# Kernel tuning notes

Hardware: AMD Instinct MI355X
Metric: run time of the kernel (lower is better)

## Reference

```python
import jax, jax.numpy as jnp
import numpy as np

DIM = 1024; NH = 16; HD = DIM // NH          # head_dim = 64
E = 8; K = 2; TEMP = 1.0; HID = 1024         # routed experts / top-k / moe_inter_dim
SHID = HID * 1                               # shared expert hidden (n_shared_experts=1)
EPS = 1e-6


def _rms(x, w):
    return x * jax.lax.rsqrt(jnp.mean(x * x, axis=-1, keepdims=True) + EPS) * w


def setup_inputs() -> dict:
    key = jax.random.key(0)
    ks = jax.random.split(key, 16)
    B, S = 2, 2048
    x = jax.random.normal(ks[0], (B, S, DIM), jnp.float32)
    # RoPE table: (S, HD//2, 2) with [..., 0]=cos, [..., 1]=sin  (theta=10000)
    inv = 1.0 / (10000.0 ** (jnp.arange(0, HD, 2, dtype=jnp.float32) / HD))
    ang = jnp.arange(S, dtype=jnp.float32)[:, None] * inv[None, :]
    freqs = jnp.stack([jnp.cos(ang), jnp.sin(ang)], axis=-1)
    sc = 0.02
    W = lambda k, shape: jax.random.normal(k, shape, jnp.float32) * sc
    return dict(
        x=x, freqs=freqs,
        att_norm_w=jnp.ones((DIM,), jnp.float32),
        wq=W(ks[1], (DIM, DIM)), wk=W(ks[2], (DIM, DIM)),
        wv=W(ks[3], (DIM, DIM)), wo=W(ks[4], (DIM, DIM)),
        ffn_norm_w=jnp.ones((DIM,), jnp.float32),
        gate_w=W(ks[5], (E, DIM)),
        ew1=W(ks[6], (E, DIM, HID)), ew2=W(ks[7], (E, HID, DIM)), ew3=W(ks[8], (E, DIM, HID)),
        sw1=W(ks[9], (DIM, SHID)), sw2=W(ks[10], (SHID, DIM)), sw3=W(ks[11], (DIM, SHID)),
    )


def reference(x, freqs, att_norm_w, wq, wk, wv, wo, ffn_norm_w, gate_w,
              ew1, ew2, ew3, sw1, sw2, sw3):
    B, S, _ = x.shape
    # --- attention sub-block ---
    xn = _rms(x, att_norm_w)
    q = (xn @ wq).reshape(B, S, NH, HD)
    k = (xn @ wk).reshape(B, S, NH, HD)
    v = (xn @ wv).reshape(B, S, NH, HD)
    cos = freqs[:S, :, 0][None, :, None, :]  # (1,S,1,HD//2)
    sin = freqs[:S, :, 1][None, :, None, :]
    def rope(t):  # complex multiply on interleaved (real, imag) pairs
        t = t.reshape(B, S, NH, HD // 2, 2)
        r = t[..., 0] * cos - t[..., 1] * sin
        i = t[..., 0] * sin + t[..., 1] * cos
        return jnp.stack([r, i], axis=-1).reshape(B, S, NH, HD)
    q = rope(q); k = rope(k)
    q = q.transpose(0, 2, 1, 3); k = k.transpose(0, 2, 1, 3); v = v.transpose(0, 2, 1, 3)
    scores = jnp.einsum('bhqd,bhkd->bhqk', q, k) / np.sqrt(HD).astype(np.float32)
    probs = jax.nn.softmax(scores.astype(jnp.float32), axis=-1).astype(q.dtype)
    att = jnp.einsum('bhqk,bhkd->bhqd', probs, v).transpose(0, 2, 1, 3).reshape(B, S, DIM)
    h = x + att @ wo
    # --- MoE sub-block ---
    hn = _rms(h, ffn_norm_w).reshape(-1, DIM)  # (N, DIM), N = B*S
    N = hn.shape[0]
    gate_scores = (hn @ gate_w.T) / TEMP
    gate_probs = jax.nn.softmax(gate_scores, axis=-1)
    topk_vals, topk_idx = jax.lax.top_k(gate_probs, K)
    # expert_mask[n, e] = routing weight (0 if not in top-k)
    expert_mask = jnp.zeros((N, E), hn.dtype).at[jnp.arange(N)[:, None], topk_idx].set(topk_vals)
    # dense grouped-GEMM form of the per-expert gather/compute/scatter loop;
    # tokens not routed to expert e get weight 0 => identical math
    h1 = jnp.einsum('nd,edh->enh', hn, ew1)
    h3 = jnp.einsum('nd,edh->enh', hn, ew3)
    eo = jnp.einsum('enh,ehd->end', jax.nn.silu(h1) * h3, ew2)
    y = jnp.einsum('end,ne->nd', eo, expert_mask)
    shared = (jax.nn.silu(hn @ sw1) * (hn @ sw3)) @ sw2
    return h + (y + shared).reshape(B, S, DIM)
```

## Files before the change

kernel.cpp:

```cpp
#include <hip/hip_runtime.h>

#define DIMD 1024
#define NHEAD 16
#define HDIM 64
#define SEQ 2048
#define NBATCH 2
#define NTOK 4096
#define NEXP 8
#define HIDD 1024
#define NSLOT 8192
#define MAXTILES 72
#define FA_BQ 128
#define FA_BK 128

typedef unsigned short ushort_t;
typedef __bf16 bf16x8 __attribute__((ext_vector_type(8)));
typedef float f32x4 __attribute__((ext_vector_type(4)));
typedef unsigned short ushort8v __attribute__((ext_vector_type(8)));
typedef unsigned short ushort4v __attribute__((ext_vector_type(4)));

#define GLL16(gp, lp) __builtin_amdgcn_global_load_lds( \
    (const __attribute__((address_space(1))) unsigned int*)(gp), \
    (__attribute__((address_space(3))) unsigned int*)(lp), 16, 0, 0)

__device__ inline float bf2f(ushort_t b) {
    union { unsigned int u; float f; } v; v.u = ((unsigned int)b) << 16; return v.f;
}
__device__ inline ushort_t f2bf(float f) {
    union { float f; unsigned int u; } v; v.f = f;
    unsigned int u = v.u;
    return (ushort_t)((u + 0x7FFFu + ((u >> 16) & 1u)) >> 16);
}
__device__ inline ushort_t cvt_bf16(float f) { return f2bf(f); }
__device__ inline ushort_t cvt_bf16(ushort_t u) { return u; }

template <typename Tin>
__global__ __launch_bounds__(256) void transpose_bf16(
    const Tin* __restrict__ in, ushort_t* __restrict__ out,
    int R, int C, int ld_in, int ld_out, int nb1,
    long si1, long si2, long so1, long so2)
{
    __shared__ ushort_t tile[32][33];
    int z = blockIdx.z, z1 = z % nb1, z2 = z / nb1;
    in  += (size_t)z1 * si1 + (size_t)z2 * si2;
    out += (size_t)z1 * so1 + (size_t)z2 * so2;
    int c0 = blockIdx.x * 32, r0 = blockIdx.y * 32;
    int tx = threadIdx.x & 31, ty = threadIdx.x >> 5;
#pragma unroll
    for (int i = 0; i < 4; i++) {
        int r = r0 + ty + i * 8, c = c0 + tx;
        ushort_t v = 0;
        if (r < R && c < C) v = cvt_bf16(in[(size_t)r * ld_in + c]);
        tile[ty + i * 8][tx] = v;
    }
    __syncthreads();
#pragma unroll
    for (int i = 0; i < 4; i++) {
        int cc = c0 + ty + i * 8, rr = r0 + tx;
        if (cc < C && rr < R) out[(size_t)cc * ld_out + rr] = tile[tx][ty + i * 8];
    }
}

__global__ __launch_bounds__(256) void rmsnorm_kernel(
    const float* __restrict__ x, const float* __restrict__ w, ushort_t* __restrict__ out)
{
    size_t row = blockIdx.x;
    const float* xr = x + row * DIMD;
    int t = threadIdx.x;
    float4 xv = ((const float4*)xr)[t];
    float ss = xv.x * xv.x + xv.y * xv.y + xv.z * xv.z + xv.w * xv.w;
    for (int o = 32; o; o >>= 1) ss += __shfl_xor(ss, o, 64);
    __shared__ float red[4];
    if ((t & 63) == 0) red[t >> 6] = ss;
    __syncthreads();
    ss = red[0] + red[1] + red[2] + red[3];
    float rs = 1.0f / sqrtf(ss / (float)DIMD + 1e-6f);
    float4 wv = ((const float4*)w)[t];
    ushort4v o;
    o[0] = f2bf(xv.x * rs * wv.x); o[1] = f2bf(xv.y * rs * wv.y);
    o[2] = f2bf(xv.z * rs * wv.z); o[3] = f2bf(xv.w * rs * wv.w);
    *(ushort4v*)(out + row * DIMD + t * 4) = o;
}

template <bool OUT_BF16, bool RESID>
__global__ __launch_bounds__(256, 2) void gemm_bt(
    const ushort_t* __restrict__ A, const ushort_t* __restrict__ B,
    void* __restrict__ Cv, const float* __restrict__ Rres,
    int M, int N, int K, int lda, int ldb, int ldc,
    int nb1, long sA1, long sA2, long sB1, long sB2, long sC1, long sC2,
    float alpha)
{
    __shared__ ushort_t lsA[128][32];
    __shared__ ushort_t lsB[128][32];
    int z = blockIdx.z, z1 = z % nb1, z2 = z / nb1;
    A += (size_t)z1 * sA1 + (size_t)z2 * sA2;
    B += (size_t)z1 * sB1 + (size_t)z2 * sB2;
    size_t coff = (size_t)z1 * sC1 + (size_t)z2 * sC2;
    int tn0 = blockIdx.x * 128, tm0 = blockIdx.y * 128;
    int t = threadIdx.x;
    int wave = t >> 6, lane = t & 63;
    int wm = (wave >> 1) * 64, wn = (wave & 1) * 64;
    int lrow = lane & 15, quad = lane >> 4;
    char* lsAb = (char*)&lsA[0][0];
    char* lsBb = (char*)&lsB[0][0];
    f32x4 acc[4][4] = {};

    for (int kt = 0; kt < K; kt += 32) {
        __syncthreads();
#pragma unroll
        for (int cc = 0; cc < 2; cc++) {
            int c = t + cc * 256;
            int r = c >> 2, kc = (c & 3) * 8;
            int ar = tm0 + r; ar = (ar < M) ? ar : (M - 1);
            GLL16(A + (size_t)ar * lda + kt + kc, lsAb + (size_t)c * 16);
            int br = tn0 + r; br = (br < N) ? br : (N - 1);
            GLL16(B + (size_t)br * ldb + kt + kc, lsBb + (size_t)c * 16);
        }
        __syncthreads();
        bf16x8 afr[4], bfr[4];
#pragma unroll
        for (int i = 0; i < 4; i++) {
            afr[i] = *(const bf16x8*)(&lsA[wm + i * 16 + lrow][quad * 8]);
            bfr[i] = *(const bf16x8*)(&lsB[wn + i * 16 + lrow][quad * 8]);
        }
#pragma unroll
        for (int mi = 0; mi < 4; mi++)
#pragma unroll
            for (int ni = 0; ni < 4; ni++)
                acc[mi][ni] = __builtin_amdgcn_mfma_f32_16x16x32_bf16(
                    afr[mi], bfr[ni], acc[mi][ni], 0, 0, 0);
    }
#pragma unroll
    for (int mi = 0; mi < 4; mi++)
#pragma unroll
        for (int ni = 0; ni < 4; ni++) {
            int col = tn0 + wn + ni * 16 + lrow;
            if (col >= N) continue;
            int row0 = tm0 + wm + mi * 16 + quad * 4;
#pragma unroll
            for (int r = 0; r < 4; r++) {
                int row = row0 + r;
                if (row >= M) continue;
                size_t idx = coff + (size_t)row * ldc + col;
                float v = acc[mi][ni][r] * alpha;
                if (RESID) v += Rres[idx];
                if (OUT_BF16) ((ushort_t*)Cv)[idx] = f2bf(v);
                else          ((float*)Cv)[idx] = v;
            }
        }
}

__global__ __launch_bounds__(256, 2) void gemm_grouped(
    const ushort_t* __restrict__ A, const ushort_t* __restrict__ Bt,
    ushort_t* __restrict__ C, const int* __restrict__ perm,
    const int* __restrict__ tile_e, const int* __restrict__ tile_r0,
    const int* __restrict__ tile_r1, const int* __restrict__ ntiles, long sBe)
{
    int tt = blockIdx.x;
    if (tt >= *ntiles) return;
    int e = tile_e[tt], r0 = tile_r0[tt], r1 = tile_r1[tt];
    const ushort_t* B = Bt + (size_t)e * sBe;
    int tn0 = blockIdx.y * 128;
    __shared__ ushort_t lsA[128][32];
    __shared__ ushort_t lsB[128][32];
    int t = threadIdx.x;
    int wave = t >> 6, lane = t & 63;
    int wm = (wave >> 1) * 64, wn = (wave & 1) * 64;
    int lrow = lane & 15, quad = lane >> 4;
    char* lsAb = (char*)&lsA[0][0];
    char* lsBb = (char*)&lsB[0][0];
    f32x4 acc[4][4] = {};

    for (int kt = 0; kt < DIMD; kt += 32) {
        __syncthreads();
#pragma unroll
        for (int cc = 0; cc < 2; cc++) {
            int c = t + cc * 256;
            int r = c >> 2, kc = (c & 3) * 8;
            int sl = r0 + r; if (sl >= r1) sl = r1 - 1;
            int ar = perm ? perm[sl] : sl;
            GLL16(A + (size_t)ar * DIMD + kt + kc, lsAb + (size_t)c * 16);
            int br = tn0 + r;
            GLL16(B + (size_t)br * DIMD + kt + kc, lsBb + (size_t)c * 16);
        }
        __syncthreads();
        bf16x8 afr[4], bfr[4];
#pragma unroll
        for (int i = 0; i < 4; i++) {
            afr[i] = *(const bf16x8*)(&lsA[wm + i * 16 + lrow][quad * 8]);
            bfr[i] = *(const bf16x8*)(&lsB[wn + i * 16 + lrow][quad * 8]);
        }
#pragma unroll
        for (int mi = 0; mi < 4; mi++)
#pragma unroll
            for (int ni = 0; ni < 4; ni++)
                acc[mi][ni] = __builtin_amdgcn_mfma_f32_16x16x32_bf16(
                    afr[mi], bfr[ni], acc[mi][ni], 0, 0, 0);
    }
#pragma unroll
    for (int mi = 0; mi < 4; mi++)
#pragma unroll
        for (int ni = 0; ni < 4; ni++) {
            int col = tn0 + wn + ni * 16 + lrow;
            int l0 = wm + mi * 16 + quad * 4;
#pragma unroll
            for (int r = 0; r < 4; r++) {
                int slot = r0 + l0 + r;
                if (slot >= r1) continue;
                C[(size_t)slot * DIMD + col] = f2bf(acc[mi][ni][r]);
            }
        }
}

__global__ __launch_bounds__(256, 2) void moe_mlp1(
    const ushort_t* __restrict__ A, const ushort_t* __restrict__ B1t, const ushort_t* __restrict__ B3t,
    ushort_t* __restrict__ C, const int* __restrict__ perm,
    const int* __restrict__ tile_e, const int* __restrict__ tile_r0,
    const int* __restrict__ tile_r1, const int* __restrict__ ntiles, long sBe)
{
    int tt = blockIdx.x;
    if (tt >= *ntiles) return;
    int e = tile_e[tt], r0 = tile_r0[tt], r1 = tile_r1[tt];
    const ushort_t* B1 = B1t + (size_t)e * sBe;
    const ushort_t* B3 = B3t + (size_t)e * sBe;
    int tn0 = blockIdx.y * 128;
    __shared__ ushort_t lsA[128][32];
    __shared__ ushort_t lsB1[128][32];
    __shared__ ushort_t lsB3[128][32];
    int t = threadIdx.x;
    int wave = t >> 6, lane = t & 63;
    int wm = (wave >> 1) * 64, wn = (wave & 1) * 64;
    int lrow = lane & 15, quad = lane >> 4;
    char* lsAb  = (char*)&lsA[0][0];
    char* lsB1b = (char*)&lsB1[0][0];
    char* lsB3b = (char*)&lsB3[0][0];
    f32x4 acc1[4][4] = {};
    f32x4 acc3[4][4] = {};

    for (int kt = 0; kt < DIMD; kt += 32) {
        __syncthreads();
#pragma unroll
        for (int cc = 0; cc < 2; cc++) {
            int c = t + cc * 256;
            int r = c >> 2, kc = (c & 3) * 8;
            int sl = r0 + r; if (sl >= r1) sl = r1 - 1;
            int ar = perm ? perm[sl] : sl;
            GLL16(A + (size_t)ar * DIMD + kt + kc, lsAb + (size_t)c * 16);
            int br = tn0 + r;
            GLL16(B1 + (size_t)br * DIMD + kt + kc, lsB1b + (size_t)c * 16);
            GLL16(B3 + (size_t)br * DIMD + kt + kc, lsB3b + (size_t)c * 16);
        }
        __syncthreads();
        bf16x8 afr[4], b1fr[4], b3fr[4];
#pragma unroll
        for (int i = 0; i < 4; i++) {
            afr[i]  = *(const bf16x8*)(&lsA[wm + i * 16 + lrow][quad * 8]);
            b1fr[i] = *(const bf16x8*)(&lsB1[wn + i * 16 + lrow][quad * 8]);
            b3fr[i] = *(const bf16x8*)(&lsB3[wn + i * 16 + lrow][quad * 8]);
        }
#pragma unroll
        for (int mi = 0; mi < 4; mi++)
#pragma unroll
            for (int ni = 0; ni < 4; ni++) {
                acc1[mi][ni] = __builtin_amdgcn_mfma_f32_16x16x32_bf16(
                    afr[mi], b1fr[ni], acc1[mi][ni], 0, 0, 0);
                acc3[mi][ni] = __builtin_amdgcn_mfma_f32_16x16x32_bf16(
                    afr[mi], b3fr[ni], acc3[mi][ni], 0, 0, 0);
            }
    }
#pragma unroll
    for (int mi = 0; mi < 4; mi++)
#pragma unroll
        for (int ni = 0; ni < 4; ni++) {
            int col = tn0 + wn + ni * 16 + lrow;
            int l0 = wm + mi * 16 + quad * 4;
#pragma unroll
            for (int r = 0; r < 4; r++) {
                int slot = r0 + l0 + r;
                if (slot >= r1) continue;
                float h1 = acc1[mi][ni][r], h3 = acc3[mi][ni][r];
                float s = h1 / (1.f + __expf(-h1));
                C[(size_t)slot * DIMD + col] = f2bf(s * h3);
            }
        }
}

__global__ __launch_bounds__(256) void rope_kernel(
    const ushort_t* __restrict__ qkv, const float* __restrict__ freqs,
    ushort_t* __restrict__ qout, ushort_t* __restrict__ kout)
{
    int s = blockIdx.x, b = blockIdx.y, t = threadIdx.x;
#pragma unroll
    for (int pp = 0; pp < 2; pp++) {
        int p = t + pp * 256;
        int hh = p >> 5, i = p & 31;
        float cs = freqs[(s * 32 + i) * 2 + 0];
        float sn = freqs[(s * 32 + i) * 2 + 1];
        size_t row = (size_t)(b * SEQ + s) * 3072;
        size_t qi = row + hh * HDIM + 2 * i;
        size_t ki = row + 1024 + hh * HDIM + 2 * i;
        size_t out_idx = ((size_t)((b * NHEAD + hh) * SEQ + s)) * HDIM + 2 * i;
        float t0 = bf2f(qkv[qi]), t1 = bf2f(qkv[qi + 1]);
        qout[out_idx]     = f2bf(t0 * cs - t1 * sn);
        qout[out_idx + 1] = f2bf(t0 * sn + t1 * cs);
        t0 = bf2f(qkv[ki]); t1 = bf2f(qkv[ki + 1]);
        kout[out_idx]     = f2bf(t0 * cs - t1 * sn);
        kout[out_idx + 1] = f2bf(t0 * sn + t1 * cs);
    }
}

__global__ __launch_bounds__(256, 2) void flash_attn(
    const ushort_t* __restrict__ q_r, const ushort_t* __restrict__ k_r,
    const ushort_t* __restrict__ vT, ushort_t* __restrict__ att)
{
    __shared__ ushort_t Kt[FA_BK][72];
    __shared__ ushort_t Vt[HDIM][136];
    __shared__ ushort_t Pt[FA_BQ][136];
    int qt = blockIdx.x, bh = blockIdx.y;
    int t = threadIdx.x, wave = t >> 6, lane = t & 63;
    int lrow = lane & 15, quad = lane >> 4;
    int qrow0 = qt * FA_BQ + wave * 32;

    const ushort_t* Qb = q_r + (size_t)bh * SEQ * HDIM;
    const ushort_t* Kb = k_r + (size_t)bh * SEQ * HDIM;
    const ushort_t* Vb = vT + (size_t)bh * HDIM * SEQ;

    bf16x8 qf[2][2];
#pragma unroll
    for (int mi = 0; mi < 2; mi++)
#pragma unroll
        for (int kk = 0; kk < 2; kk++)
            qf[mi][kk] = *(const bf16x8*)(Qb + (size_t)(qrow0 + mi * 16 + lrow) * HDIM + kk * 32 + quad * 8);

    f32x4 Oacc[2][4] = {};
    float mst[2][4], lst[2][4];
#pragma unroll
    for (int mi = 0; mi < 2; mi++)
#pragma unroll
        for (int r = 0; r < 4; r++) { mst[mi][r] = -3e38f; lst[mi][r] = 0.f; }

    for (int kc = 0; kc < SEQ / FA_BK; kc++) {
        __syncthreads();
#pragma unroll
        for (int p = 0; p < 4; p++) {
            int c = t + p * 256;
            int r = c >> 3, j = c & 7;
            *(ushort8v*)(&Kt[r][j * 8]) =
                *(const ushort8v*)(Kb + (size_t)(kc * FA_BK + r) * HDIM + j * 8);
        }
#pragma unroll
        for (int p = 0; p < 4; p++) {
            int c = t + p * 256;
            int r = c >> 4, j = c & 15;
            *(ushort8v*)(&Vt[r][j * 8]) =
                *(const ushort8v*)(Vb + (size_t)r * SEQ + kc * FA_BK + j * 8);
        }
        __syncthreads();
        f32x4 s[2][8] = {};
#pragma unroll
        for (int nj = 0; nj < 8; nj++) {
            bf16x8 bf0 = *(const bf16x8*)(&Kt[nj * 16 + lrow][quad * 8]);
            bf16x8 bf1 = *(const bf16x8*)(&Kt[nj * 16 + lrow][32 + quad * 8]);
#pragma unroll
            for (int mi = 0; mi < 2; mi++) {
                s[mi][nj] = __builtin_amdgcn_mfma_f32_16x16x32_bf16(qf[mi][0], bf0, s[mi][nj], 0, 0, 0);
                s[mi][nj] = __builtin_amdgcn_mfma_f32_16x16x32_bf16(qf[mi][1], bf1, s[mi][nj], 0, 0, 0);
            }
        }
#pragma unroll
        for (int mi = 0; mi < 2; mi++)
#pragma unroll
            for (int r = 0; r < 4; r++) {
                float rowmax = -3e38f;
#pragma unroll
                for (int nj = 0; nj < 8; nj++) rowmax = fmaxf(rowmax, s[mi][nj][r]);
                rowmax *= 0.125f;
#pragma unroll
                for (int o = 1; o < 16; o <<= 1) rowmax = fmaxf(rowmax, __shfl_xor(rowmax, o, 64));
                float mnew = fmaxf(mst[mi][r], rowmax);
                float alpha = __expf(mst[mi][r] - mnew);
                float rsum = 0.f;
#pragma unroll
                for (int nj = 0; nj < 8; nj++) {
                    float pv = __expf(s[mi][nj][r] * 0.125f - mnew);
                    s[mi][nj][r] = pv;
                    rsum += pv;
                }
#pragma unroll
                for (int o = 1; o < 16; o <<= 1) rsum += __shfl_xor(rsum, o, 64);
                lst[mi][r] = lst[mi][r] * alpha + rsum;
                mst[mi][r] = mnew;
#pragma unroll
                for (int nj = 0; nj < 4; nj++) Oacc[mi][nj][r] *= alpha;
            }
#pragma unroll
        for (int mi = 0; mi < 2; mi++)
#pragma unroll
            for (int nj = 0; nj < 8; nj++)
#pragma unroll
                for (int r = 0; r < 4; r++)
                    Pt[wave * 32 + mi * 16 + quad * 4 + r][nj * 16 + lrow] = f2bf(s[mi][nj][r]);
#pragma unroll
        for (int kk = 0; kk < 4; kk++) {
            bf16x8 af0 = *(const bf16x8*)(&Pt[wave * 32 + lrow][kk * 32 + quad * 8]);
            bf16x8 af1 = *(const bf16x8*)(&Pt[wave * 32 + 16 + lrow][kk * 32 + quad * 8]);
#pragma unroll
            for (int nj = 0; nj < 4; nj++) {
                bf16x8 bf = *(const bf16x8*)(&Vt[nj * 16 + lrow][kk * 32 + quad * 8]);
                Oacc[0][nj] = __builtin_amdgcn_mfma_f32_16x16x32_bf16(af0, bf, Oacc[0][nj], 0, 0, 0);
                Oacc[1][nj] = __builtin_amdgcn_mfma_f32_16x16x32_bf16(af1, bf, Oacc[1][nj], 0, 0, 0);
            }
        }
    }
    int b = bh >> 4, h = bh & 15;
#pragma unroll
    for (int mi = 0; mi < 2; mi++)
#pragma unroll
        for (int r = 0; r < 4; r++) {
            int srow = qrow0 + mi * 16 + quad * 4 + r;
            float inv = 1.0f / lst[mi][r];
#pragma unroll
            for (int nj = 0; nj < 4; nj++) {
                int d = nj * 16 + lrow;
                att[((size_t)(b * SEQ + srow)) * DIMD + h * HDIM + d] = f2bf(Oacc[mi][nj][r] * inv);
            }
        }
}

__global__ __launch_bounds__(256) void gate_kernel(
    const float* __restrict__ h, const float* __restrict__ gw, const float* __restrict__ fw,
    int* __restrict__ tok_e, float* __restrict__ tok_w)
{
    int tok = blockIdx.x, t = threadIdx.x;
    const float* hr = h + (size_t)tok * DIMD;
    float ssq = 0.f;
    for (int k = t; k < DIMD; k += 256) { float v = hr[k]; ssq += v * v; }
    for (int o = 32; o; o >>= 1) ssq += __shfl_xor(ssq, o, 64);
    __shared__ float red[4];
    if ((t & 63) == 0) red[t >> 6] = ssq;
    __syncthreads();
    ssq = red[0] + red[1] + red[2] + red[3];
    float rs = 1.0f / sqrtf(ssq / (float)DIMD + 1e-6f);
    int e = t >> 5, lane = t & 31;
    float sc = 0.f;
    for (int k = lane; k < DIMD; k += 32) sc += hr[k] * rs * fw[k] * gw[e * DIMD + k];
    for (int o = 16; o; o >>= 1) sc += __shfl_down(sc, o, 32);
    __shared__ float se[NEXP];
    if (lane == 0) se[e] = sc;
    __syncthreads();
    if (t == 0) {
        float mx = se[0];
        for (int i = 1; i < NEXP; i++) mx = fmaxf(mx, se[i]);
        float pr[NEXP], sum = 0.f;
        for (int i = 0; i < NEXP; i++) { pr[i] = __expf(se[i] - mx); sum += pr[i]; }
        float inv = 1.0f / sum;
        for (int i = 0; i < NEXP; i++) pr[i] *= inv;
        int i0 = 0;
        for (int i = 1; i < NEXP; i++) if (pr[i] > pr[i0]) i0 = i;
        int i1 = -1;
        for (int i = 0; i < NEXP; i++) { if (i == i0) continue; if (i1 < 0 || pr[i] > pr[i1]) i1 = i; }
        tok_e[tok * 2] = i0; tok_e[tok * 2 + 1] = i1;
        tok_w[tok * 2] = pr[i0]; tok_w[tok * 2 + 1] = pr[i1];
    }
}

__global__ __launch_bounds__(1024) void route_kernel(
    const int* __restrict__ tok_e, int* __restrict__ ntiles,
    int* __restrict__ tile_e, int* __restrict__ tile_r0, int* __restrict__ tile_r1,
    int* __restrict__ perm, int* __restrict__ slot_of)
{
    __shared__ int hist[NEXP][1024];
    __shared__ int totals[NEXP], offs[NEXP];
    int t = threadIdx.x;
    int e_loc[8];
    int c[NEXP];
#pragma unroll
    for (int e = 0; e < NEXP; e++) c[e] = 0;
#pragma unroll
    for (int j = 0; j < 8; j++) { int e = tok_e[t * 8 + j]; e_loc[j] = e; c[e]++; }
#pragma unroll
    for (int e = 0; e < NEXP; e++) hist[e][t] = c[e];
    __syncthreads();
    int wv = t >> 6, ln = t & 63;
    if (wv < NEXP) {
        int run = 0;
        for (int ch = 0; ch < 16; ch++) {
            int v = hist[wv][ch * 64 + ln];
            int x = v;
#pragma unroll
            for (int o = 1; o < 64; o <<= 1) { int y = __shfl_up(x, o, 64); if (ln >= o) x += y; }
            hist[wv][ch * 64 + ln] = run + x - v;
            run += __shfl(x, 63, 64);
        }
        if (ln == 0) totals[wv] = run;
    }
    __syncthreads();
    if (t == 0) {
        int off = 0, nt = 0;
        for (int e = 0; e < NEXP; e++) {
            offs[e] = off;
            int cc = totals[e];
            for (int r = 0; r < cc; r += 128) {
                tile_e[nt] = e;
                tile_r0[nt] = off + r;
                tile_r1[nt] = off + ((r + 128 < cc) ? (r + 128) : cc);
                nt++;
            }
            off += cc;
        }
        *ntiles = nt;
    }
    __syncthreads();
    int c2[NEXP];
#pragma unroll
    for (int e = 0; e < NEXP; e++) c2[e] = 0;
#pragma unroll
    for (int j = 0; j < 8; j++) {
        int e = e_loc[j];
        int slot = offs[e] + hist[e][t] + c2[e]++;
        perm[slot] = (t * 8 + j) >> 1;
        slot_of[t * 8 + j] = slot;
    }
}

__global__ __launch_bounds__(256) void silu_pair(
    const ushort_t* __restrict__ s13, ushort_t* __restrict__ o)
{
    int i = blockIdx.x * 256 + threadIdx.x;
    int stride = gridDim.x * 256;
    for (; i < NTOK * DIMD; i += stride) {
        int r = i >> 10, c = i & 1023;
        float a = bf2f(s13[(size_t)r * 2048 + c]);
        float b = bf2f(s13[(size_t)r * 2048 + 1024 + c]);
        o[i] = f2bf(a / (1.f + __expf(-a)) * b);
    }
}

__global__ __launch_bounds__(256) void combine_kernel(
    const float* __restrict__ shf, const ushort_t* __restrict__ eo,
    const int* __restrict__ slot_of, const float* __restrict__ tok_w, float* __restrict__ out)
{
    int tok = blockIdx.x, t = threadIdx.x;
    int s0 = slot_of[tok * 2], s1 = slot_of[tok * 2 + 1];
    float w0 = tok_w[tok * 2], w1 = tok_w[tok * 2 + 1];
    const ushort_t* e0 = eo + (size_t)s0 * DIMD;
    const ushort_t* e1 = eo + (size_t)s1 * DIMD;
    size_t base = (size_t)tok * DIMD;
    for (int k = t; k < DIMD; k += 256)
        out[base + k] = shf[base + k] + w0 * bf2f(e0[k]) + w1 * bf2f(e1[k]);
}

__global__ void report_ws(float* out, float v) { out[0] = v; }

extern "C" void kernel_launch(void* const* d_in, const int* in_sizes, int n_in,
                              void* d_out, int out_size, void* d_ws, size_t ws_size,
                              hipStream_t stream)
{
    const float* x     = (const float*)d_in[0];
    const float* freqs = (const float*)d_in[1];
    const float* attw  = (const float*)d_in[2];
    const float* wq    = (const float*)d_in[3];
    const float* wk    = (const float*)d_in[4];
    const float* wv    = (const float*)d_in[5];
    const float* wo    = (const float*)d_in[6];
    const float* ffnw  = (const float*)d_in[7];
    const float* gatew = (const float*)d_in[8];
    const float* ew1   = (const float*)d_in[9];
    const float* ew2   = (const float*)d_in[10];
    const float* ew3   = (const float*)d_in[11];
    const float* sw1   = (const float*)d_in[12];
    const float* sw2   = (const float*)d_in[13];
    const float* sw3   = (const float*)d_in[14];
    float* out = (float*)d_out;

    char* ws = (char*)d_ws;
    const size_t MB = 1024 * 1024;
    const size_t MM = (size_t)DIMD * DIMD;
    if (ws_size < 160 * MB) { report_ws<<<1, 1, 0, stream>>>(out, (float)ws_size); return; }

    ushort_t* wqT  = (ushort_t*)(ws + 0 * MB);
    ushort_t* wkT  = (ushort_t*)(ws + 2 * MB);
    ushort_t* wvT  = (ushort_t*)(ws + 4 * MB);
    ushort_t* woT  = (ushort_t*)(ws + 6 * MB);
    ushort_t* sw1T = (ushort_t*)(ws + 8 * MB);
    ushort_t* sw3T = (ushort_t*)(ws + 10 * MB);
    ushort_t* sw2T = (ushort_t*)(ws + 12 * MB);
    ushort_t* ew1T = (ushort_t*)(ws + 14 * MB);
    ushort_t* ew2T = (ushort_t*)(ws + 30 * MB);
    ushort_t* ew3T = (ushort_t*)(ws + 46 * MB);
    float*    hbuf = (float*)   (ws + 62 * MB);
    ushort_t* hn   = (ushort_t*)(ws + 78 * MB);
    ushort_t* actb = (ushort_t*)(ws + 86 * MB);
    ushort_t* eo   = (ushort_t*)(ws + 102 * MB);
    ushort_t* xn   = (ushort_t*)(ws + 86 * MB);
    ushort_t* qkv  = (ushort_t*)(ws + 94 * MB);
    ushort_t* q_r  = (ushort_t*)(ws + 118 * MB);
    ushort_t* k_r  = (ushort_t*)(ws + 126 * MB);
    ushort_t* vTb  = (ushort_t*)(ws + 134 * MB);
    ushort_t* att  = (ushort_t*)(ws + 142 * MB);
    ushort_t* s13  = (ushort_t*)(ws + 118 * MB);
    ushort_t* shb  = (ushort_t*)(ws + 134 * MB);
    float*    shf  = (float*)   (ws + 142 * MB);
    int*      meta = (int*)     (ws + 158 * MB);

    int* ntiles  = meta;
    int* tile_e  = meta + 32;     int* tile_r0 = meta + 104;  int* tile_r1 = meta + 176;
    int* tok_e   = meta + 256;    int* slot_of = meta + 256 + 8192;
    int* permv   = meta + 256 + 16384;
    float* tok_w = (float*)(meta + 256 + 24576);

    transpose_bf16<float><<<dim3(32, 32, 1), 256, 0, stream>>>(wq,  wqT,  DIMD, DIMD, DIMD, DIMD, 1, 0, 0, 0, 0);
    transpose_bf16<float><<<dim3(32, 32, 1), 256, 0, stream>>>(wk,  wkT,  DIMD, DIMD, DIMD, DIMD, 1, 0, 0, 0, 0);
    transpose_bf16<float><<<dim3(32, 32, 1), 256, 0, stream>>>(wv,  wvT,  DIMD, DIMD, DIMD, DIMD, 1, 0, 0, 0, 0);
    transpose_bf16<float><<<dim3(32, 32, 1), 256, 0, stream>>>(wo,  woT,  DIMD, DIMD, DIMD, DIMD, 1, 0, 0, 0, 0);
    transpose_bf16<float><<<dim3(32, 32, 1), 256, 0, stream>>>(sw1, sw1T, DIMD, DIMD, DIMD, DIMD, 1, 0, 0, 0, 0);
    transpose_bf16<float><<<dim3(32, 32, 1), 256, 0, stream>>>(sw3, sw3T, DIMD, DIMD, DIMD, DIMD, 1, 0, 0, 0, 0);
    transpose_bf16<float><<<dim3(32, 32, 1), 256, 0, stream>>>(sw2, sw2T, DIMD, DIMD, DIMD, DIMD, 1, 0, 0, 0, 0);
    transpose_bf16<float><<<dim3(32, 32, 8), 256, 0, stream>>>(ew1, ew1T, DIMD, DIMD, DIMD, DIMD, 8, (long)MM, 0, (long)MM, 0);
    transpose_bf16<float><<<dim3(32, 32, 8), 256, 0, stream>>>(ew2, ew2T, DIMD, DIMD, DIMD, DIMD, 8, (long)MM, 0, (long)MM, 0);
    transpose_bf16<float><<<dim3(32, 32, 8), 256, 0, stream>>>(ew3, ew3T, DIMD, DIMD, DIMD, DIMD, 8, (long)MM, 0, (long)MM, 0);

    rmsnorm_kernel<<<NTOK, 256, 0, stream>>>(x, attw, xn);
    gemm_bt<true, false><<<dim3(24, 32, 1), 256, 0, stream>>>(xn, wqT, qkv, nullptr,
        NTOK, 3072, DIMD, DIMD, DIMD, 3072, 1, 0, 0, 0, 0, 0, 0, 1.0f);
    rope_kernel<<<dim3(SEQ, NBATCH), 256, 0, stream>>>(qkv, freqs, q_r, k_r);
    transpose_bf16<ushort_t><<<dim3(HDIM / 32, SEQ / 32, NBATCH * NHEAD), 256, 0, stream>>>(
        qkv + 2048, vTb, SEQ, HDIM, 3072, SEQ, NHEAD,
        (long)HDIM, (long)SEQ * 3072, (long)HDIM * SEQ, (long)NHEAD * HDIM * SEQ);

    flash_attn<<<dim3(SEQ / FA_BQ, NBATCH * NHEAD), 256, 0, stream>>>(q_r, k_r, vTb, att);

    gemm_bt<false, true><<<dim3(8, 32, 1), 256, 0, stream>>>(att, woT, hbuf, x,
        NTOK, DIMD, DIMD, DIMD, DIMD, DIMD, 1, 0, 0, 0, 0, 0, 0, 1.0f);
    rmsnorm_kernel<<<NTOK, 256, 0, stream>>>(hbuf, ffnw, hn);

    gate_kernel<<<NTOK, 256, 0, stream>>>(hbuf, gatew, ffnw, tok_e, tok_w);
    route_kernel<<<1, 1024, 0, stream>>>(tok_e, ntiles, tile_e, tile_r0, tile_r1, permv, slot_of);

    moe_mlp1<<<dim3(MAXTILES, 8), 256, 0, stream>>>(hn, ew1T, ew3T, actb, permv,
        tile_e, tile_r0, tile_r1, ntiles, (long)MM);
    gemm_grouped<<<dim3(MAXTILES, 8), 256, 0, stream>>>(actb, ew2T, eo, nullptr,
        tile_e, tile_r0, tile_r1, ntiles, (long)MM);

    gemm_bt<true, false><<<dim3(16, 32, 1), 256, 0, stream>>>(hn, sw1T, s13, nullptr,
        NTOK, 2048, DIMD, DIMD, DIMD, 2048, 1, 0, 0, 0, 0, 0, 0, 1.0f);
    silu_pair<<<2048, 256, 0, stream>>>(s13, shb);
    gemm_bt<false, true><<<dim3(8, 32, 1), 256, 0, stream>>>(shb, sw2T, shf, hbuf,
        NTOK, DIMD, DIMD, DIMD, DIMD, DIMD, 1, 0, 0, 0, 0, 0, 0, 1.0f);

    combine_kernel<<<NTOK, 256, 0, stream>>>(shf, eo, slot_of, tok_w, out);
}
```

Baseline: 678.8 us.

## Shrink flash-attn key tile, use exp2, merge weight transposes, swap MoE grid axes

Flash attention now uses 64-key tiles with smaller LDS buffers and a launch bound of 4 waves per SIMD, so more blocks fit per CU. Softmax uses exp2 with pre-folded log2e scaling. Seven separate weight transpose launches become one launch of a new multi-source kernel. The MoE grouped GEMMs swap grid axes so the column-tile index is fastest, which should improve reuse of the A rows. The trade-off is twice as many K iterations and syncs in attention, plus tighter register pressure.

```diff
diff --git a/kernel.cpp b/kernel.cpp
--- a/kernel.cpp
+++ b/kernel.cpp
@@ -11,7 +11,7 @@
 #define NSLOT 8192
 #define MAXTILES 72
 #define FA_BQ 128
-#define FA_BK 128
+#define FA_BK 64
 
 typedef unsigned short ushort_t;
 typedef __bf16 bf16x8 __attribute__((ext_vector_type(8)));
@@ -59,6 +59,26 @@
         int cc = c0 + ty + i * 8, rr = r0 + tx;
         if (cc < C && rr < R) out[(size_t)cc * ld_out + rr] = tile[tx][ty + i * 8];
     }
+}
+
+__global__ __launch_bounds__(256) void transpose7(
+    const float* __restrict__ p0, const float* __restrict__ p1, const float* __restrict__ p2,
+    const float* __restrict__ p3, const float* __restrict__ p4, const float* __restrict__ p5,
+    const float* __restrict__ p6, ushort_t* __restrict__ out)
+{
+    __shared__ ushort_t tile[32][33];
+    const float* srcs[7] = {p0, p1, p2, p3, p4, p5, p6};
+    const float* in = srcs[blockIdx.z];
+    ushort_t* o = out + (size_t)blockIdx.z * DIMD * DIMD;
+    int c0 = blockIdx.x * 32, r0 = blockIdx.y * 32;
+    int tx = threadIdx.x & 31, ty = threadIdx.x >> 5;
+#pragma unroll
+    for (int i = 0; i < 4; i++)
+        tile[ty + i * 8][tx] = f2bf(in[(size_t)(r0 + ty + i * 8) * DIMD + c0 + tx]);
+    __syncthreads();
+#pragma unroll
+    for (int i = 0; i < 4; i++)
+        o[(size_t)(c0 + ty + i * 8) * DIMD + r0 + tx] = tile[tx][ty + i * 8];
 }
 
 __global__ __launch_bounds__(256) void rmsnorm_kernel(
@@ -156,11 +176,11 @@
     const int* __restrict__ tile_e, const int* __restrict__ tile_r0,
     const int* __restrict__ tile_r1, const int* __restrict__ ntiles, long sBe)
 {
-    int tt = blockIdx.x;
+    int tt = blockIdx.y;
     if (tt >= *ntiles) return;
     int e = tile_e[tt], r0 = tile_r0[tt], r1 = tile_r1[tt];
     const ushort_t* B = Bt + (size_t)e * sBe;
-    int tn0 = blockIdx.y * 128;
+    int tn0 = blockIdx.x * 128;
     __shared__ ushort_t lsA[128][32];
     __shared__ ushort_t lsB[128][32];
     int t = threadIdx.x;
@@ -218,12 +238,12 @@
     const int* __restrict__ tile_e, const int* __restrict__ tile_r0,
     const int* __restrict__ tile_r1, const int* __restrict__ ntiles, long sBe)
 {
-    int tt = blockIdx.x;
+    int tt = blockIdx.y;
     if (tt >= *ntiles) return;
     int e = tile_e[tt], r0 = tile_r0[tt], r1 = tile_r1[tt];
     const ushort_t* B1 = B1t + (size_t)e * sBe;
     const ushort_t* B3 = B3t + (size_t)e * sBe;
-    int tn0 = blockIdx.y * 128;
+    int tn0 = blockIdx.x * 128;
     __shared__ ushort_t lsA[128][32];
     __shared__ ushort_t lsB1[128][32];
     __shared__ ushort_t lsB3[128][32];
@@ -309,17 +329,19 @@
     }
 }
 
-__global__ __launch_bounds__(256, 2) void flash_attn(
+__global__ __launch_bounds__(256, 4) void flash_attn(
     const ushort_t* __restrict__ q_r, const ushort_t* __restrict__ k_r,
     const ushort_t* __restrict__ vT, ushort_t* __restrict__ att)
 {
     __shared__ ushort_t Kt[FA_BK][72];
-    __shared__ ushort_t Vt[HDIM][136];
-    __shared__ ushort_t Pt[FA_BQ][136];
+    __shared__ ushort_t Vt[HDIM][72];
+    __shared__ ushort_t Pt[FA_BQ][72];
     int qt = blockIdx.x, bh = blockIdx.y;
     int t = threadIdx.x, wave = t >> 6, lane = t & 63;
     int lrow = lane & 15, quad = lane >> 4;
     int qrow0 = qt * FA_BQ + wave * 32;
+    const float S2 = 0.18033688f;
+    const float M2 = 1.44269504f;
 
     const ushort_t* Qb = q_r + (size_t)bh * SEQ * HDIM;
     const ushort_t* Kb = k_r + (size_t)bh * SEQ * HDIM;
@@ -342,23 +364,23 @@
     for (int kc = 0; kc < SEQ / FA_BK; kc++) {
         __syncthreads();
 #pragma unroll
-        for (int p = 0; p < 4; p++) {
+        for (int p = 0; p < 2; p++) {
             int c = t + p * 256;
             int r = c >> 3, j = c & 7;
             *(ushort8v*)(&Kt[r][j * 8]) =
                 *(const ushort8v*)(Kb + (size_t)(kc * FA_BK + r) * HDIM + j * 8);
         }
 #pragma unroll
-        for (int p = 0; p < 4; p++) {
+        for (int p = 0; p < 2; p++) {
             int c = t + p * 256;
-            int r = c >> 4, j = c & 15;
+            int r = c >> 3, j = c & 7;
             *(ushort8v*)(&Vt[r][j * 8]) =
                 *(const ushort8v*)(Vb + (size_t)r * SEQ + kc * FA_BK + j * 8);
         }
         __syncthreads();
-        f32x4 s[2][8] = {};
-#pragma unroll
-        for (int nj = 0; nj < 8; nj++) {
+        f32x4 s[2][4] = {};
+#pragma unroll
+        for (int nj = 0; nj < 4; nj++) {
             bf16x8 bf0 = *(const bf16x8*)(&Kt[nj * 16 + lrow][quad * 8]);
             bf16x8 bf1 = *(const bf16x8*)(&Kt[nj * 16 + lrow][32 + quad * 8]);
 #pragma unroll
@@ -371,18 +393,17 @@
         for (int mi = 0; mi < 2; mi++)
 #pragma unroll
             for (int r = 0; r < 4; r++) {
-                float rowmax = -3e38f;
-#pragma unroll
-                for (int nj = 0; nj < 8; nj++) rowmax = fmaxf(rowmax, s[mi][nj][r]);
+                float rowmax = fmaxf(fmaxf(s[mi][0][r], s[mi][1][r]), fmaxf(s[mi][2][r], s[mi][3][r]));
                 rowmax *= 0.125f;
 #pragma unroll
                 for (int o = 1; o < 16; o <<= 1) rowmax = fmaxf(rowmax, __shfl_xor(rowmax, o, 64));
                 float mnew = fmaxf(mst[mi][r], rowmax);
-                float alpha = __expf(mst[mi][r] - mnew);
+                float alpha = __builtin_amdgcn_exp2f(M2 * (mst[mi][r] - mnew));
+                float mb = M2 * mnew;
                 float rsum = 0.f;
 #pragma unroll
-                for (int nj = 0; nj < 8; nj++) {
-                    float pv = __expf(s[mi][nj][r] * 0.125f - mnew);
+                for (int nj = 0; nj < 4; nj++) {
+                    float pv = __builtin_amdgcn_exp2f(s[mi][nj][r] * S2 - mb);
                     s[mi][nj][r] = pv;
                     rsum += pv;
                 }
@@ -396,12 +417,12 @@
 #pragma unroll
         for (int mi = 0; mi < 2; mi++)
 #pragma unroll
-            for (int nj = 0; nj < 8; nj++)
+            for (int nj = 0; nj < 4; nj++)
 #pragma unroll
                 for (int r = 0; r < 4; r++)
                     Pt[wave * 32 + mi * 16 + quad * 4 + r][nj * 16 + lrow] = f2bf(s[mi][nj][r]);
 #pragma unroll
-        for (int kk = 0; kk < 4; kk++) {
+        for (int kk = 0; kk < 2; kk++) {
             bf16x8 af0 = *(const bf16x8*)(&Pt[wave * 32 + lrow][kk * 32 + quad * 8]);
             bf16x8 af1 = *(const bf16x8*)(&Pt[wave * 32 + 16 + lrow][kk * 32 + quad * 8]);
 #pragma unroll
@@ -579,11 +600,8 @@
     if (ws_size < 160 * MB) { report_ws<<<1, 1, 0, stream>>>(out, (float)ws_size); return; }
 
     ushort_t* wqT  = (ushort_t*)(ws + 0 * MB);
-    ushort_t* wkT  = (ushort_t*)(ws + 2 * MB);
-    ushort_t* wvT  = (ushort_t*)(ws + 4 * MB);
     ushort_t* woT  = (ushort_t*)(ws + 6 * MB);
     ushort_t* sw1T = (ushort_t*)(ws + 8 * MB);
-    ushort_t* sw3T = (ushort_t*)(ws + 10 * MB);
     ushort_t* sw2T = (ushort_t*)(ws + 12 * MB);
     ushort_t* ew1T = (ushort_t*)(ws + 14 * MB);
     ushort_t* ew2T = (ushort_t*)(ws + 30 * MB);
@@ -609,13 +627,7 @@
     int* permv   = meta + 256 + 16384;
     float* tok_w = (float*)(meta + 256 + 24576);
 
-    transpose_bf16<float><<<dim3(32, 32, 1), 256, 0, stream>>>(wq,  wqT,  DIMD, DIMD, DIMD, DIMD, 1, 0, 0, 0, 0);
-    transpose_bf16<float><<<dim3(32, 32, 1), 256, 0, stream>>>(wk,  wkT,  DIMD, DIMD, DIMD, DIMD, 1, 0, 0, 0, 0);
-    transpose_bf16<float><<<dim3(32, 32, 1), 256, 0, stream>>>(wv,  wvT,  DIMD, DIMD, DIMD, DIMD, 1, 0, 0, 0, 0);
-    transpose_bf16<float><<<dim3(32, 32, 1), 256, 0, stream>>>(wo,  woT,  DIMD, DIMD, DIMD, DIMD, 1, 0, 0, 0, 0);
-    transpose_bf16<float><<<dim3(32, 32, 1), 256, 0, stream>>>(sw1, sw1T, DIMD, DIMD, DIMD, DIMD, 1, 0, 0, 0, 0);
-    transpose_bf16<float><<<dim3(32, 32, 1), 256, 0, stream>>>(sw3, sw3T, DIMD, DIMD, DIMD, DIMD, 1, 0, 0, 0, 0);
-    transpose_bf16<float><<<dim3(32, 32, 1), 256, 0, stream>>>(sw2, sw2T, DIMD, DIMD, DIMD, DIMD, 1, 0, 0, 0, 0);
+    transpose7<<<dim3(32, 32, 7), 256, 0, stream>>>(wq, wk, wv, wo, sw1, sw3, sw2, wqT);
     transpose_bf16<float><<<dim3(32, 32, 8), 256, 0, stream>>>(ew1, ew1T, DIMD, DIMD, DIMD, DIMD, 8, (long)MM, 0, (long)MM, 0);
     transpose_bf16<float><<<dim3(32, 32, 8), 256, 0, stream>>>(ew2, ew2T, DIMD, DIMD, DIMD, DIMD, 8, (long)MM, 0, (long)MM, 0);
     transpose_bf16<float><<<dim3(32, 32, 8), 256, 0, stream>>>(ew3, ew3T, DIMD, DIMD, DIMD, DIMD, 8, (long)MM, 0, (long)MM, 0);
@@ -637,9 +649,9 @@
     gate_kernel<<<NTOK, 256, 0, stream>>>(hbuf, gatew, ffnw, tok_e, tok_w);
     route_kernel<<<1, 1024, 0, stream>>>(tok_e, ntiles, tile_e, tile_r0, tile_r1, permv, slot_of);
 
-    moe_mlp1<<<dim3(MAXTILES, 8), 256, 0, stream>>>(hn, ew1T, ew3T, actb, permv,
+    moe_mlp1<<<dim3(8, MAXTILES), 256, 0, stream>>>(hn, ew1T, ew3T, actb, permv,
         tile_e, tile_r0, tile_r1, ntiles, (long)MM);
-    gemm_grouped<<<dim3(MAXTILES, 8), 256, 0, stream>>>(actb, ew2T, eo, nullptr,
+    gemm_grouped<<<dim3(8, MAXTILES), 256, 0, stream>>>(actb, ew2T, eo, nullptr,
         tile_e, tile_r0, tile_r1, ntiles, (long)MM);
 
     gemm_bt<true, false><<<dim3(16, 32, 1), 256, 0, stream>>>(hn, sw1T, s13, nullptr,
```

Measured after the change: 708.9 us. 4.4% more time.
